# Performance work log

Hardware: AMD Instinct MI355X
Metric: run time of the kernel (lower is better)

## Reference

```python
import jax, jax.numpy as jnp
import numpy as np

B, T, N, H, F, E = 8, 64, 2048, 64, 64, 32768
G = 3 * H  # GRU gate dim


def setup_inputs() -> dict:
    key = jax.random.key(0)
    ks = jax.random.split(key, 12)
    s = 0.05
    return {
        "x": jax.random.normal(ks[0], (B, T, N, F), jnp.float32),
        "targets": jax.random.normal(ks[1], (B, T, N, 1), jnp.float32),
        "targets_mask": jax.random.uniform(ks[2], (B, T, N, 1)) > 0.2,
        "edge_index": jax.random.randint(ks[3], (2, E), 0, N),
        "W_msg": jax.random.normal(ks[4], (H, H), jnp.float32) * s,
        "b_msg": jnp.zeros((H,), jnp.float32),
        "W_mix": jax.random.normal(ks[5], (H, H + F), jnp.float32) * s,
        "b_mix": jnp.zeros((H,), jnp.float32),
        "W_ih": jax.random.normal(ks[6], (N, G, H), jnp.float32) * s,
        "W_hh": jax.random.normal(ks[7], (N, G, H), jnp.float32) * s,
        "b_ih": jnp.zeros((N, G), jnp.float32),
        "b_hh": jnp.zeros((N, G), jnp.float32),
        "W_read": jax.random.normal(ks[8], (1, H), jnp.float32) * s,
        "b_read": jnp.zeros((1,), jnp.float32),
    }


def reference(x, targets, targets_mask, edge_index,
              W_msg, b_msg, W_mix, b_mix,
              W_ih, W_hh, b_ih, b_hh, W_read, b_read):
    src, dst = edge_index[0], edge_index[1]

    def step(state, x_t):
        # state: [B,N,H], x_t: [B,N,F]
        m = jnp.einsum('bnh,gh->bng', state, W_msg) + b_msg           # state_to_message
        agg = jnp.zeros_like(m).at[:, dst, :].add(m[:, src, :])       # add-aggregate over directed edges
        mi = jnp.concatenate([agg, x_t], axis=-1)                     # [B,N,H+F]
        m2 = jnp.einsum('bnf,hf->bnh', mi, W_mix) + b_mix             # mix_input
        # per-node independent GRU cells (batched weights [N,3H,*])
        gi = jnp.einsum('bnh,ngh->bng', m2, W_ih) + b_ih
        gh = jnp.einsum('bnh,ngh->bng', state, W_hh) + b_hh
        i_r, i_z, i_n = jnp.split(gi, 3, axis=-1)
        h_r, h_z, h_n = jnp.split(gh, 3, axis=-1)
        r = jax.nn.sigmoid(i_r + h_r)
        z = jax.nn.sigmoid(i_z + h_z)
        n_cand = jnp.tanh(i_n + r * h_n)
        new_state = (1.0 - z) * n_cand + z * state
        out = jnp.einsum('bnh,oh->bno', new_state, W_read) + b_read   # readout -> [B,N,1]
        return new_state, out

    state0 = jnp.zeros((B, N, H), x.dtype)
    _, outs = jax.lax.scan(step, state0, jnp.swapaxes(x, 0, 1))       # outs: [T,B,N,1]
    outputs = jnp.swapaxes(outs, 0, 1)                                # [B,T,N,1]
    loss = 0.5 * (outputs - targets) ** 2
    mask = targets_mask.astype(loss.dtype)
    return jnp.sum(loss * mask) / jnp.sum(mask)                       # masked mean
```

## Files before the change

kernel.cpp:

```cpp
#include <hip/hip_runtime.h>
#include <math.h>

namespace {
constexpr int B = 8, T = 64, N = 2048, H = 64, F = 64, E = 32768, G = 192;
constexpr int BNH = B * N * H;
constexpr int NWELEM = N * G * H;
constexpr int NBLK = 1024;
}

typedef __attribute__((ext_vector_type(8))) short bfrag;
typedef __attribute__((ext_vector_type(4))) float ffrag;
typedef long f8frag;

#define MFMA(a, b, c)  __builtin_amdgcn_mfma_f32_16x16x32_bf16(a, b, c, 0, 0, 0)
#define MFMA8(a, b, c) __builtin_amdgcn_mfma_f32_16x16x32_fp8_fp8(a, b, c, 0, 0, 0)

#define DS (1.f / 512.f)

__device__ __forceinline__ unsigned short f2bf(float f) {
  unsigned u = __float_as_uint(f);
  u += 0x7fffu + ((u >> 16) & 1u);
  return (unsigned short)(u >> 16);
}
__device__ __forceinline__ float bf2f(unsigned short u) {
  return __uint_as_float(((unsigned)u) << 16);
}
template<bool HI>
__device__ __forceinline__ unsigned cvtpk8(float a, float b, unsigned old) {
  return __builtin_amdgcn_cvt_pk_fp8_f32(a, b, old, HI);
}

__device__ __forceinline__ void grid_bar(int* bar, int t) {
  __syncthreads();
  if (threadIdx.x == 0) {
    __threadfence();
    int old = __hip_atomic_fetch_add(&bar[(blockIdx.x & 63) * 64], 1,
                                     __ATOMIC_RELAXED, __HIP_MEMORY_SCOPE_AGENT);
    if ((old & 15) == 15) {
      int old2 = __hip_atomic_fetch_add(&bar[4096], 1,
                                        __ATOMIC_RELAXED, __HIP_MEMORY_SCOPE_AGENT);
      if ((old2 & 63) == 63)
        __hip_atomic_fetch_add(&bar[4160], 1, __ATOMIC_RELAXED, __HIP_MEMORY_SCOPE_AGENT);
    }
    while (__hip_atomic_load(&bar[4160], __ATOMIC_RELAXED, __HIP_MEMORY_SCOPE_AGENT) <= t)
      __builtin_amdgcn_s_sleep(8);
    __threadfence();
  }
  __syncthreads();
}


__global__ __launch_bounds__(256) void init_kernel(
    float* __restrict__ state, unsigned short* __restrict__ mA,
    const float* __restrict__ b_msg, float* __restrict__ loss_acc,
    float* __restrict__ scal, int* __restrict__ deg, int* __restrict__ bar)
{
  int stride = gridDim.x * blockDim.x;
  for (int i = blockIdx.x * blockDim.x + threadIdx.x; i < BNH; i += stride) {
    state[i] = 0.f;
    mA[i] = f2bf(b_msg[i & (H - 1)]);
    if (i < 8192) bar[i] = 0;
    if (i < N) { loss_acc[i] = 0.f; deg[i] = 0; }
    if (i < 16) scal[i] = 0.f;
  }
}

__global__ __launch_bounds__(256) void conv_kernel(
    const float* __restrict__ Wi, const float* __restrict__ Wh,
    const float* __restrict__ Wm, const float* __restrict__ Wg,
    unsigned char* __restrict__ Wib, unsigned char* __restrict__ Whb,
    unsigned short* __restrict__ Wmb, unsigned short* __restrict__ Wgb)
{
  int stride = gridDim.x * blockDim.x * 2;
  for (int i = (blockIdx.x * blockDim.x + threadIdx.x) * 2; i < NWELEM; i += stride) {
    unsigned p = cvtpk8<false>(Wi[i] * 32.f, Wi[i + 1] * 32.f, 0u);
    *(unsigned short*)(Wib + i) = (unsigned short)p;
    p = cvtpk8<false>(Wh[i] * 32.f, Wh[i + 1] * 32.f, 0u);
    *(unsigned short*)(Whb + i) = (unsigned short)p;
    if (i < 64 * 128) { Wmb[i] = f2bf(Wm[i]); Wmb[i + 1] = f2bf(Wm[i + 1]); }
    if (i < 64 * 64)  { Wgb[i] = f2bf(Wg[i]); Wgb[i + 1] = f2bf(Wg[i + 1]); }
  }
}

__global__ __launch_bounds__(256) void hist_kernel(const int* __restrict__ ei, int* __restrict__ deg) {
  int e = blockIdx.x * 256 + threadIdx.x;
  if (e < E) atomicAdd(&deg[ei[E + e]], 1);
}

__global__ __launch_bounds__(1024) void scan_kernel(const int* __restrict__ deg,
    int* __restrict__ row_ptr, int* __restrict__ cursor)
{
  __shared__ int s[N];
  int tid = threadIdx.x;
  s[tid] = deg[tid];
  s[tid + 1024] = deg[tid + 1024];
  __syncthreads();
  for (int off = 1; off < N; off <<= 1) {
    int v0 = (tid >= off) ? s[tid - off] : 0;
    int v1 = s[tid + 1024 - off];
    __syncthreads();
    s[tid] += v0;
    s[tid + 1024] += v1;
    __syncthreads();
  }
  row_ptr[tid + 1] = s[tid];
  row_ptr[tid + 1025] = s[tid + 1024];
  cursor[tid] = (tid == 0) ? 0 : s[tid - 1];
  cursor[tid + 1024] = s[tid + 1023];
  if (tid == 0) row_ptr[0] = 0;
}

__global__ __launch_bounds__(256) void fill_kernel(const int* __restrict__ ei,
    int* __restrict__ cursor, int* __restrict__ col_src)
{
  int e = blockIdx.x * 256 + threadIdx.x;
  if (e < E) {
    int d = ei[E + e];
    int slot = atomicAdd(&cursor[d], 1);
    col_src[slot] = ei[e];
  }
}

__global__ __launch_bounds__(256) void mask_kernel(const int* __restrict__ mask, float* __restrict__ scal) {
  int stride = gridDim.x * blockDim.x;
  int v = 0;
  for (int i = blockIdx.x * blockDim.x + threadIdx.x; i < B * T * N; i += stride)
    v += (mask[i] != 0);
  for (int o = 1; o < 64; o <<= 1) v += __shfl_xor(v, o, 64);
  if ((threadIdx.x & 63) == 0) atomicAdd(&scal[0], (float)v);
}


__global__ __attribute__((amdgpu_flat_work_group_size(256, 256), amdgpu_waves_per_eu(4, 4)))
void persist_kernel(
    const float* __restrict__ x, const float* __restrict__ targets,
    const int* __restrict__ mask,
    const unsigned char* __restrict__ W_ihb, const unsigned char* __restrict__ W_hhb,
    const unsigned short* __restrict__ W_mixb, const unsigned short* __restrict__ W_msgb,
    const float* __restrict__ b_ih, const float* __restrict__ b_hh,
    const float* __restrict__ b_mix, const float* __restrict__ b_msg,
    const float* __restrict__ W_read, const float* __restrict__ b_read,
    const int* __restrict__ row_ptr, const int* __restrict__ col_src,
    unsigned short* __restrict__ mAb, unsigned short* __restrict__ mBb,
    float* __restrict__ loss_acc, int* __restrict__ bar)
{
  __shared__ float sts[2][8][64];
  __shared__ float partial[4][8][72];
  __shared__ unsigned char m2F8[8 * 80];
  __shared__ unsigned short nsA[8 * 72];
  __shared__ float redS[4][8];

  const int tid = threadIdx.x;
  const int w = tid >> 6, lane = tid & 63;
  const int mrow = lane & 15, quad = lane >> 4;
  const int n0 = blockIdx.x * 2;
  const bfrag za = (bfrag)0;
  const int hcol = w * 16 + mrow;

  f8frag whf[2][6], wif[2][6];
#pragma unroll
  for (int k = 0; k < 2; ++k) {
    const unsigned char* Wh = W_hhb + (size_t)(n0 + k) * (G * H);
    const unsigned char* Wi = W_ihb + (size_t)(n0 + k) * (G * H);
#pragma unroll
    for (int tt = 0; tt < 3; ++tt) {
      const int off = ((w + tt * 4) * 16 + mrow) * H + quad * 8;
      whf[k][2 * tt]     = *(const f8frag*)(Wh + off);
      whf[k][2 * tt + 1] = *(const f8frag*)(Wh + off + 32);
      wif[k][2 * tt]     = *(const f8frag*)(Wi + off);
      wif[k][2 * tt + 1] = *(const f8frag*)(Wi + off + 32);
    }
  }
  const unsigned short* wmp = W_mixb + hcol * 128 + quad * 8;
  const unsigned short* wgp = W_msgb + hcol * H + quad * 8;

  float bir[2], biz[2], bin_[2], bhr[2], bhz[2], bhn[2];
#pragma unroll
  for (int k = 0; k < 2; ++k) {
    const int bg = (n0 + k) * G + hcol;
    bir[k] = b_ih[bg]; biz[k] = b_ih[bg + 64]; bin_[k] = b_ih[bg + 128];
    bhr[k] = b_hh[bg]; bhz[k] = b_hh[bg + 64]; bhn[k] = b_hh[bg + 128];
  }
  float wrd = W_read[hcol];
  float bmix = b_mix[hcol];
  float bmsg = b_msg[hcol];
  const float brd = b_read[0];
  const int e0a = row_ptr[n0], e0b = row_ptr[n0 + 1], e0c = row_ptr[n0 + 2];

#pragma unroll
  for (int k = 0; k < 2; ++k) {
#pragma unroll
    for (int j = 0; j < 6; ++j) {
      asm volatile("" : "+v"(whf[k][j]));
      asm volatile("" : "+v"(wif[k][j]));
    }
    asm volatile("" : "+v"(bir[k]), "+v"(biz[k]), "+v"(bin_[k]),
                      "+v"(bhr[k]), "+v"(bhz[k]), "+v"(bhn[k]));
  }
  asm volatile("" : "+v"(wrd), "+v"(bmix), "+v"(bmsg));

  for (int i = tid; i < 2 * 8 * 64; i += 256) ((float*)sts)[i] = 0.f;
  __syncthreads();

  float lsum[2] = {0.f, 0.f};
  unsigned short* mcur = mAb;
  unsigned short* mnxt = mBb;

#pragma unroll 1
  for (int t = 0; t < T; ++t) {
#pragma unroll
    for (int k = 0; k < 2; ++k) {
      const int nn = n0 + k;
      const int ee0 = k ? e0b : e0a;
      const int ee1 = k ? e0c : e0b;

      bfrag wm0 = *(const bfrag*)(wmp);
      bfrag wm1 = *(const bfrag*)(wmp + 32);
      bfrag wm2 = *(const bfrag*)(wmp + 64);
      bfrag wm3 = *(const bfrag*)(wmp + 96);
      f8frag asF0 = 0, asF1 = 0;
      bfrag a2 = za, a3 = za;
      if (mrow < 8) {
        const float* sp = &sts[k][mrow][0];
        {
          float4 s0 = *(const float4*)(sp + quad * 8);
          float4 s1 = *(const float4*)(sp + quad * 8 + 4);
          unsigned u0 = 0, u1 = 0;
          u0 = cvtpk8<false>(s0.x * 16.f, s0.y * 16.f, u0);
          u0 = cvtpk8<true >(s0.z * 16.f, s0.w * 16.f, u0);
          u1 = cvtpk8<false>(s1.x * 16.f, s1.y * 16.f, u1);
          u1 = cvtpk8<true >(s1.z * 16.f, s1.w * 16.f, u1);
          asF0 = (f8frag)(((unsigned long long)u1 << 32) | u0);
          s0 = *(const float4*)(sp + 32 + quad * 8);
          s1 = *(const float4*)(sp + 32 + quad * 8 + 4);
          u0 = 0; u1 = 0;
          u0 = cvtpk8<false>(s0.x * 16.f, s0.y * 16.f, u0);
          u0 = cvtpk8<true >(s0.z * 16.f, s0.w * 16.f, u0);
          u1 = cvtpk8<false>(s1.x * 16.f, s1.y * 16.f, u1);
          u1 = cvtpk8<true >(s1.z * 16.f, s1.w * 16.f, u1);
          asF1 = (f8frag)(((unsigned long long)u1 << 32) | u0);
        }
        const float* xp = x + (((size_t)mrow * T + t) * N + nn) * F;
        {
          float4 t0 = *(const float4*)(xp + quad * 8);
          float4 t1 = *(const float4*)(xp + quad * 8 + 4);
          a2[0]=(short)f2bf(t0.x); a2[1]=(short)f2bf(t0.y); a2[2]=(short)f2bf(t0.z); a2[3]=(short)f2bf(t0.w);
          a2[4]=(short)f2bf(t1.x); a2[5]=(short)f2bf(t1.y); a2[6]=(short)f2bf(t1.z); a2[7]=(short)f2bf(t1.w);
          t0 = *(const float4*)(xp + 32 + quad * 8);
          t1 = *(const float4*)(xp + 32 + quad * 8 + 4);
          a3[0]=(short)f2bf(t0.x); a3[1]=(short)f2bf(t0.y); a3[2]=(short)f2bf(t0.z); a3[3]=(short)f2bf(t0.w);
          a3[4]=(short)f2bf(t1.x); a3[5]=(short)f2bf(t1.y); a3[6]=(short)f2bf(t1.z); a3[7]=(short)f2bf(t1.w);
        }
      }
      {
        float acc[8] = {0.f,0.f,0.f,0.f,0.f,0.f,0.f,0.f};
#pragma unroll 2
        for (int e = ee0 + w; e < ee1; e += 4) {
          const unsigned short* mp = mcur + (size_t)col_src[e] * (B * H) + lane;
#pragma unroll
          for (int b = 0; b < 8; ++b) acc[b] += bf2f(mp[b * H]);
        }
#pragma unroll
        for (int b = 0; b < 8; ++b) partial[w][b][lane] = acc[b];
      }
      ffrag ah0 = {0.f,0.f,0.f,0.f}, ah1 = {0.f,0.f,0.f,0.f}, ah2 = {0.f,0.f,0.f,0.f};
      ah0 = MFMA8(asF0, whf[k][0], ah0); ah0 = MFMA8(asF1, whf[k][1], ah0);
      ah1 = MFMA8(asF0, whf[k][2], ah1); ah1 = MFMA8(asF1, whf[k][3], ah1);
      ah2 = MFMA8(asF0, whf[k][4], ah2); ah2 = MFMA8(asF1, whf[k][5], ah2);
      __syncthreads();

      {
        bfrag a0 = za, a1 = za;
        if (mrow < 8) {
          const float* p = &partial[0][mrow][quad * 8];
#pragma unroll
          for (int j = 0; j < 8; ++j) {
            float s = p[j] + p[j + 576] + p[j + 1152] + p[j + 1728];
            a0[j] = (short)f2bf(s);
          }
          const float* p2 = &partial[0][mrow][32 + quad * 8];
#pragma unroll
          for (int j = 0; j < 8; ++j) {
            float s = p2[j] + p2[j + 576] + p2[j + 1152] + p2[j + 1728];
            a1[j] = (short)f2bf(s);
          }
        }
        ffrag accm = {0.f, 0.f, 0.f, 0.f};
        accm = MFMA(a0, wm0, accm);
        accm = MFMA(a1, wm1, accm);
        accm = MFMA(a2, wm2, accm);
        accm = MFMA(a3, wm3, accm);
        if (quad < 2) {
#pragma unroll
          for (int r = 0; r < 4; ++r) {
            unsigned p = cvtpk8<false>((accm[r] + bmix) * 16.f, 0.f, 0u);
            m2F8[(quad * 4 + r) * 80 + hcol] = (unsigned char)(p & 0xffu);
          }
        }
      }
      __syncthreads();

      bfrag wg0 = *(const bfrag*)(wgp);
      bfrag wg1 = *(const bfrag*)(wgp + 32);
      {
        f8frag amF0 = 0, amF1 = 0;
        if (mrow < 8) {
          amF0 = *(const f8frag*)&m2F8[mrow * 80 + quad * 8];
          amF1 = *(const f8frag*)&m2F8[mrow * 80 + 32 + quad * 8];
        }
        ffrag ai0 = {0.f,0.f,0.f,0.f}, ai1 = {0.f,0.f,0.f,0.f}, ai2 = {0.f,0.f,0.f,0.f};
        ai0 = MFMA8(amF0, wif[k][0], ai0); ai0 = MFMA8(amF1, wif[k][1], ai0);
        ai1 = MFMA8(amF0, wif[k][2], ai1); ai1 = MFMA8(amF1, wif[k][3], ai1);
        ai2 = MFMA8(amF0, wif[k][4], ai2); ai2 = MFMA8(amF1, wif[k][5], ai2);
        if (quad < 2) {
          float v[4];
#pragma unroll
          for (int r = 0; r < 4; ++r) {
            const int b = quad * 4 + r;
            float rs  = (ai0[r] + ah0[r]) * DS + bir[k] + bhr[k];
            float zs  = (ai1[r] + ah1[r]) * DS + biz[k] + bhz[k];
            float in_ = ai2[r] * DS + bin_[k];
            float hn  = ah2[r] * DS + bhn[k];
            float rg = 1.f / (1.f + __expf(-rs));
            float z  = 1.f / (1.f + __expf(-zs));
            float pre = in_ + rg * hn;
            float a = __expf(-2.f * fabsf(pre));
            float nc = copysignf((1.f - a) / (1.f + a), pre);
            float sold = sts[k][b][hcol];
            float ns = (1.f - z) * nc + z * sold;
            sts[k][b][hcol] = ns;
            nsA[b * 72 + hcol] = f2bf(ns);
            v[r] = ns * wrd;
          }
#pragma unroll
          for (int o = 1; o < 16; o <<= 1) {
#pragma unroll
            for (int r = 0; r < 4; ++r) v[r] += __shfl_xor(v[r], o, 64);
          }
          if (mrow == 0) {
#pragma unroll
            for (int r = 0; r < 4; ++r) redS[w][quad * 4 + r] = v[r];
          }
        }
      }
      __syncthreads();

      {
        bfrag an0 = za, an1 = za;
        if (mrow < 8) {
          an0 = *(const bfrag*)&nsA[mrow * 72 + quad * 8];
          an1 = *(const bfrag*)&nsA[mrow * 72 + 32 + quad * 8];
        }
        ffrag accg = {0.f, 0.f, 0.f, 0.f};
        accg = MFMA(an0, wg0, accg);
        accg = MFMA(an1, wg1, accg);
        if (quad < 2) {
#pragma unroll
          for (int r = 0; r < 4; ++r)
            mnxt[(size_t)nn * (B * H) + (quad * 4 + r) * H + hcol] = f2bf(accg[r] + bmsg);
        }
      }
      if (tid < 8) {
        float vv = redS[0][tid] + redS[1][tid] + redS[2][tid] + redS[3][tid] + brd;
        size_t idx = ((size_t)tid * T + t) * N + nn;
        float d = vv - targets[idx];
        float l = (mask[idx] != 0) ? 0.5f * d * d : 0.f;
        l += __shfl_xor(l, 1, 64);
        l += __shfl_xor(l, 2, 64);
        l += __shfl_xor(l, 4, 64);
        if (tid == 0) lsum[k] += l;
      }
    }
    grid_bar(bar, t);
    unsigned short* tp = mcur; mcur = mnxt; mnxt = tp;
  }
  if (tid == 0) { loss_acc[n0] = lsum[0]; loss_acc[n0 + 1] = lsum[1]; }
}


__global__ __launch_bounds__(256, 4) void step_kernel(
    const float* __restrict__ x, const float* __restrict__ targets,
    const int* __restrict__ mask, float* __restrict__ state,
    const unsigned char* __restrict__ W_ihb, const unsigned char* __restrict__ W_hhb,
    const unsigned short* __restrict__ W_mixb, const unsigned short* __restrict__ W_msgb,
    const float* __restrict__ b_ih, const float* __restrict__ b_hh,
    const float* __restrict__ b_mix, const float* __restrict__ b_msg,
    const float* __restrict__ W_read, const float* __restrict__ b_read,
    const int* __restrict__ row_ptr, const int* __restrict__ col_src,
    const unsigned short* __restrict__ m_cur, unsigned short* __restrict__ m_nxt,
    float* __restrict__ loss_acc, int t)
{
  __shared__ float partial[4][8][72];
  __shared__ unsigned char m2F8[8 * 80];
  __shared__ unsigned short nsA[8 * 72];
  __shared__ float redS[4][8];

  const int n = blockIdx.x;
  const int tid = threadIdx.x;
  const int w = tid >> 6, lane = tid & 63;
  const int mrow = lane & 15, quad = lane >> 4;
  const bfrag za = (bfrag)0;

  f8frag whf[6];
  {
    const unsigned char* Wh = W_hhb + (size_t)n * (G * H);
#pragma unroll
    for (int tt = 0; tt < 3; ++tt) {
      const unsigned char* wrh = Wh + (((w + tt * 4) * 16 + mrow) * H) + quad * 8;
      whf[2 * tt]     = *(const f8frag*)(wrh);
      whf[2 * tt + 1] = *(const f8frag*)(wrh + 32);
    }
  }
  f8frag asF0 = 0, asF1 = 0;
  float4 xv0 = {0.f,0.f,0.f,0.f}, xv1 = {0.f,0.f,0.f,0.f};
  float4 xv2 = {0.f,0.f,0.f,0.f}, xv3 = {0.f,0.f,0.f,0.f};
  if (mrow < 8) {
    const float* sp = state + (size_t)n * (B * H) + mrow * H;
    float4 s0 = *(const float4*)(sp + quad * 8);
    float4 s1 = *(const float4*)(sp + quad * 8 + 4);
    float4 s2 = *(const float4*)(sp + 32 + quad * 8);
    float4 s3 = *(const float4*)(sp + 32 + quad * 8 + 4);
    unsigned u0 = 0, u1 = 0;
    u0 = cvtpk8<false>(s0.x * 16.f, s0.y * 16.f, u0);
    u0 = cvtpk8<true >(s0.z * 16.f, s0.w * 16.f, u0);
    u1 = cvtpk8<false>(s1.x * 16.f, s1.y * 16.f, u1);
    u1 = cvtpk8<true >(s1.z * 16.f, s1.w * 16.f, u1);
    asF0 = (f8frag)(((unsigned long long)u1 << 32) | u0);
    u0 = 0; u1 = 0;
    u0 = cvtpk8<false>(s2.x * 16.f, s2.y * 16.f, u0);
    u0 = cvtpk8<true >(s2.z * 16.f, s2.w * 16.f, u0);
    u1 = cvtpk8<false>(s3.x * 16.f, s3.y * 16.f, u1);
    u1 = cvtpk8<true >(s3.z * 16.f, s3.w * 16.f, u1);
    asF1 = (f8frag)(((unsigned long long)u1 << 32) | u0);
    const float* xp = x + (((size_t)mrow * T + t) * N + n) * F;
    xv0 = *(const float4*)(xp + quad * 8);
    xv1 = *(const float4*)(xp + quad * 8 + 4);
    xv2 = *(const float4*)(xp + 32 + quad * 8);
    xv3 = *(const float4*)(xp + 32 + quad * 8 + 4);
  }
  {
    float acc[8] = {0.f,0.f,0.f,0.f,0.f,0.f,0.f,0.f};
    const int e0 = row_ptr[n], e1 = row_ptr[n + 1];
#pragma unroll 2
    for (int e = e0 + w; e < e1; e += 4) {
      const unsigned short* mp = m_cur + (size_t)col_src[e] * (B * H) + lane;
#pragma unroll
      for (int b = 0; b < 8; ++b) acc[b] += bf2f(mp[b * H]);
    }
#pragma unroll
    for (int b = 0; b < 8; ++b) partial[w][b][lane] = acc[b];
  }
  ffrag ah0 = {0.f,0.f,0.f,0.f}, ah1 = {0.f,0.f,0.f,0.f}, ah2 = {0.f,0.f,0.f,0.f};
  ah0 = MFMA8(asF0, whf[0], ah0); ah0 = MFMA8(asF1, whf[1], ah0);
  ah1 = MFMA8(asF0, whf[2], ah1); ah1 = MFMA8(asF1, whf[3], ah1);
  ah2 = MFMA8(asF0, whf[4], ah2); ah2 = MFMA8(asF1, whf[5], ah2);
  __syncthreads();

  f8frag wif[6];
  {
    const unsigned char* Wi = W_ihb + (size_t)n * (G * H);
#pragma unroll
    for (int tt = 0; tt < 3; ++tt) {
      const unsigned char* wri = Wi + (((w + tt * 4) * 16 + mrow) * H) + quad * 8;
      wif[2 * tt]     = *(const f8frag*)(wri);
      wif[2 * tt + 1] = *(const f8frag*)(wri + 32);
    }
  }
  {
    const int g0 = w * 16;
    bfrag a0 = za, a1 = za, a2 = za, a3 = za;
    if (mrow < 8) {
      const float* p = &partial[0][mrow][quad * 8];
#pragma unroll
      for (int j = 0; j < 8; ++j) {
        float s = p[j] + p[j + 576] + p[j + 1152] + p[j + 1728];
        a0[j] = (short)f2bf(s);
      }
      const float* p2 = &partial[0][mrow][32 + quad * 8];
#pragma unroll
      for (int j = 0; j < 8; ++j) {
        float s = p2[j] + p2[j + 576] + p2[j + 1152] + p2[j + 1728];
        a1[j] = (short)f2bf(s);
      }
      a2[0]=(short)f2bf(xv0.x); a2[1]=(short)f2bf(xv0.y); a2[2]=(short)f2bf(xv0.z); a2[3]=(short)f2bf(xv0.w);
      a2[4]=(short)f2bf(xv1.x); a2[5]=(short)f2bf(xv1.y); a2[6]=(short)f2bf(xv1.z); a2[7]=(short)f2bf(xv1.w);
      a3[0]=(short)f2bf(xv2.x); a3[1]=(short)f2bf(xv2.y); a3[2]=(short)f2bf(xv2.z); a3[3]=(short)f2bf(xv2.w);
      a3[4]=(short)f2bf(xv3.x); a3[5]=(short)f2bf(xv3.y); a3[6]=(short)f2bf(xv3.z); a3[7]=(short)f2bf(xv3.w);
    }
    const unsigned short* wm = W_mixb + (g0 + mrow) * 128 + quad * 8;
    ffrag accm = {0.f, 0.f, 0.f, 0.f};
    accm = MFMA(a0, *(const bfrag*)(wm), accm);
    accm = MFMA(a1, *(const bfrag*)(wm + 32), accm);
    accm = MFMA(a2, *(const bfrag*)(wm + 64), accm);
    accm = MFMA(a3, *(const bfrag*)(wm + 96), accm);
    if (quad < 2) {
      float bm = b_mix[g0 + mrow];
#pragma unroll
      for (int r = 0; r < 4; ++r) {
        unsigned p = cvtpk8<false>((accm[r] + bm) * 16.f, 0.f, 0u);
        m2F8[(quad * 4 + r) * 80 + g0 + mrow] = (unsigned char)(p & 0xffu);
      }
    }
  }
  __syncthreads();

  {
    f8frag amF0 = 0, amF1 = 0;
    if (mrow < 8) {
      amF0 = *(const f8frag*)&m2F8[mrow * 80 + quad * 8];
      amF1 = *(const f8frag*)&m2F8[mrow * 80 + 32 + quad * 8];
    }
    ffrag ai0 = {0.f,0.f,0.f,0.f}, ai1 = {0.f,0.f,0.f,0.f}, ai2 = {0.f,0.f,0.f,0.f};
    ai0 = MFMA8(amF0, wif[0], ai0); ai0 = MFMA8(amF1, wif[1], ai0);
    ai1 = MFMA8(amF0, wif[2], ai1); ai1 = MFMA8(amF1, wif[3], ai1);
    ai2 = MFMA8(amF0, wif[4], ai2); ai2 = MFMA8(amF1, wif[5], ai2);
    if (quad < 2) {
      const int hcol = w * 16 + mrow;
      const int bg = n * G + hcol;
      const float bir = b_ih[bg], biz = b_ih[bg + 64], bin_ = b_ih[bg + 128];
      const float bhr = b_hh[bg], bhz = b_hh[bg + 64], bhn = b_hh[bg + 128];
      const float wrd = W_read[hcol];
      float v[4];
#pragma unroll
      for (int r = 0; r < 4; ++r) {
        const int b = quad * 4 + r;
        float rs  = (ai0[r] + ah0[r]) * DS + bir + bhr;
        float zs  = (ai1[r] + ah1[r]) * DS + biz + bhz;
        float in_ = ai2[r] * DS + bin_;
        float hn  = ah2[r] * DS + bhn;
        float rg = 1.f / (1.f + __expf(-rs));
        float z  = 1.f / (1.f + __expf(-zs));
        float pre = in_ + rg * hn;
        float a = __expf(-2.f * fabsf(pre));
        float nc = copysignf((1.f - a) / (1.f + a), pre);
        float sold = state[(size_t)n * (B * H) + b * H + hcol];
        float ns = (1.f - z) * nc + z * sold;
        state[(size_t)n * (B * H) + b * H + hcol] = ns;
        nsA[b * 72 + hcol] = f2bf(ns);
        v[r] = ns * wrd;
      }
#pragma unroll
      for (int o = 1; o < 16; o <<= 1) {
#pragma unroll
        for (int r = 0; r < 4; ++r) v[r] += __shfl_xor(v[r], o, 64);
      }
      if (mrow == 0) {
#pragma unroll
        for (int r = 0; r < 4; ++r) redS[w][quad * 4 + r] = v[r];
      }
    }
  }
  __syncthreads();

  {
    const int g0 = w * 16;
    bfrag an0 = za, an1 = za;
    if (mrow < 8) {
      an0 = *(const bfrag*)&nsA[mrow * 72 + quad * 8];
      an1 = *(const bfrag*)&nsA[mrow * 72 + 32 + quad * 8];
    }
    const unsigned short* wg = W_msgb + (g0 + mrow) * H + quad * 8;
    ffrag accg = {0.f, 0.f, 0.f, 0.f};
    accg = MFMA(an0, *(const bfrag*)(wg), accg);
    accg = MFMA(an1, *(const bfrag*)(wg + 32), accg);
    if (quad < 2) {
      float bm = b_msg[g0 + mrow];
#pragma unroll
      for (int r = 0; r < 4; ++r)
        m_nxt[(size_t)n * (B * H) + (quad * 4 + r) * H + g0 + mrow] = f2bf(accg[r] + bm);
    }
  }
  if (tid < 8) {
    float vv = redS[0][tid] + redS[1][tid] + redS[2][tid] + redS[3][tid] + b_read[0];
    size_t idx = ((size_t)tid * T + t) * N + n;
    float d = vv - targets[idx];
    float l = (mask[idx] != 0) ? 0.5f * d * d : 0.f;
    l += __shfl_xor(l, 1, 64);
    l += __shfl_xor(l, 2, 64);
    l += __shfl_xor(l, 4, 64);
    if (tid == 0) loss_acc[n] += l;
  }
}

__global__ __launch_bounds__(256) void final_kernel(const float* __restrict__ loss_acc,
    const float* __restrict__ scal, float* __restrict__ out)
{
  __shared__ float sred[4];
  float v = 0.f;
  for (int i = threadIdx.x; i < N; i += 256) v += loss_acc[i];
  for (int o = 1; o < 64; o <<= 1) v += __shfl_xor(v, o, 64);
  if ((threadIdx.x & 63) == 0) sred[threadIdx.x >> 6] = v;
  __syncthreads();
  if (threadIdx.x == 0) out[0] = (sred[0] + sred[1] + sred[2] + sred[3]) / scal[0];
}

extern "C" void kernel_launch(void* const* d_in, const int* in_sizes, int n_in,
                              void* d_out, int out_size, void* d_ws, size_t ws_size,
                              hipStream_t stream)
{
  const float* x       = (const float*)d_in[0];
  const float* targets = (const float*)d_in[1];
  const int*   mask    = (const int*)d_in[2];
  const int*   ei      = (const int*)d_in[3];
  const float* W_msg   = (const float*)d_in[4];
  const float* b_msg   = (const float*)d_in[5];
  const float* W_mix   = (const float*)d_in[6];
  const float* b_mix   = (const float*)d_in[7];
  const float* W_ih    = (const float*)d_in[8];
  const float* W_hh    = (const float*)d_in[9];
  const float* b_ih    = (const float*)d_in[10];
  const float* b_hh    = (const float*)d_in[11];
  const float* W_read  = (const float*)d_in[12];
  const float* b_read  = (const float*)d_in[13];
  float* out = (float*)d_out;

  float* state          = (float*)d_ws;
  unsigned short* mA    = (unsigned short*)(state + BNH);
  unsigned short* mB    = mA + BNH;
  float* loss_acc       = (float*)(mB + BNH);
  float* scal           = loss_acc + N;
  int* deg              = (int*)(scal + 16);
  int* row_ptr          = deg + N;
  int* cursor           = row_ptr + (N + 16);
  int* col_src          = cursor + N;
  int* bar              = col_src + E;
  unsigned char* W_ihb  = (unsigned char*)(bar + 8192);
  unsigned char* W_hhb  = W_ihb + NWELEM;
  unsigned short* W_mixb = (unsigned short*)(W_hhb + NWELEM);
  unsigned short* W_msgb = W_mixb + 64 * 128;

  init_kernel<<<1024, 256, 0, stream>>>(state, mA, b_msg, loss_acc, scal, deg, bar);
  conv_kernel<<<8192, 256, 0, stream>>>(W_ih, W_hh, W_mix, W_msg, W_ihb, W_hhb, W_mixb, W_msgb);
  hist_kernel<<<E / 256, 256, 0, stream>>>(ei, deg);
  scan_kernel<<<1, 1024, 0, stream>>>(deg, row_ptr, cursor);
  fill_kernel<<<E / 256, 256, 0, stream>>>(ei, cursor, col_src);
  mask_kernel<<<512, 256, 0, stream>>>(mask, scal);

  int dev = 0, ncu = 0, occ = 0;
  hipGetDevice(&dev);
  hipDeviceGetAttribute(&ncu, hipDeviceAttributeMultiprocessorCount, dev);
  hipOccupancyMaxActiveBlocksPerMultiprocessor(&occ, (const void*)persist_kernel, 256, 0);
  const bool use_persist = ((long)occ * ncu >= NBLK);

  if (use_persist) {
    persist_kernel<<<NBLK, 256, 0, stream>>>(x, targets, mask,
                                             W_ihb, W_hhb, W_mixb, W_msgb,
                                             b_ih, b_hh, b_mix, b_msg, W_read, b_read,
                                             row_ptr, col_src, mA, mB, loss_acc, bar);
  } else {
    unsigned short* mcur = mA;
    unsigned short* mnxt = mB;
    for (int t = 0; t < T; ++t) {
      step_kernel<<<N, 256, 0, stream>>>(x, targets, mask, state,
                                         W_ihb, W_hhb, W_mixb, W_msgb,
                                         b_ih, b_hh, b_mix, b_msg, W_read, b_read,
                                         row_ptr, col_src, mcur, mnxt, loss_acc, t);
      unsigned short* tmp = mcur; mcur = mnxt; mnxt = tmp;
    }
  }
  final_kernel<<<1, 256, 0, stream>>>(loss_acc, scal, out);
}
```

Measured before the change: 2.223 ms.

## Replace hierarchical grid barrier with master-block barrier and packed atomic message accesses

Replaces the tree-style atomic grid barrier, which used thread fences and a two-level counter, with release-ordered per-slot counters. Block 0 polls all 64 slots and publishes a single generation flag, which the other blocks spin on with short sleeps. Message gather and scatter now use 32-bit packed bf16 pairs through relaxed agent-scope atomic loads and stores, presumably so the data stays coherent without full fences and with fewer, wider memory accesses. This risks weaker memory-ordering guarantees, since there is no acquire fence after the wait, and adds a serial polling step in block 0.

New measurement: 2.221 ms. No clear change (-0.1%).

```diff
diff --git a/kernel.cpp b/kernel.cpp
--- a/kernel.cpp
+++ b/kernel.cpp
@@ -33,18 +33,20 @@
 __device__ __forceinline__ void grid_bar(int* bar, int t) {
   __syncthreads();
   if (threadIdx.x == 0) {
-    __threadfence();
-    int old = __hip_atomic_fetch_add(&bar[(blockIdx.x & 63) * 64], 1,
-                                     __ATOMIC_RELAXED, __HIP_MEMORY_SCOPE_AGENT);
-    if ((old & 15) == 15) {
-      int old2 = __hip_atomic_fetch_add(&bar[4096], 1,
-                                        __ATOMIC_RELAXED, __HIP_MEMORY_SCOPE_AGENT);
-      if ((old2 & 63) == 63)
-        __hip_atomic_fetch_add(&bar[4160], 1, __ATOMIC_RELAXED, __HIP_MEMORY_SCOPE_AGENT);
-    }
-    while (__hip_atomic_load(&bar[4160], __ATOMIC_RELAXED, __HIP_MEMORY_SCOPE_AGENT) <= t)
-      __builtin_amdgcn_s_sleep(8);
-    __threadfence();
+    __hip_atomic_fetch_add(&bar[(blockIdx.x & 63) * 16], 1,
+                           __ATOMIC_RELEASE, __HIP_MEMORY_SCOPE_AGENT);
+  }
+  if (blockIdx.x == 0) {
+    if (threadIdx.x < 64) {
+      while (__hip_atomic_load(&bar[threadIdx.x * 16],
+                               __ATOMIC_RELAXED, __HIP_MEMORY_SCOPE_AGENT) < 16 * (t + 1))
+        __builtin_amdgcn_s_sleep(1);
+      if (threadIdx.x == 0)
+        __hip_atomic_store(&bar[4096], t + 1, __ATOMIC_RELAXED, __HIP_MEMORY_SCOPE_AGENT);
+    }
+  } else if (threadIdx.x == 0) {
+    while (__hip_atomic_load(&bar[4096], __ATOMIC_RELAXED, __HIP_MEMORY_SCOPE_AGENT) < t + 1)
+      __builtin_amdgcn_s_sleep(2);
   }
   __syncthreads();
 }
@@ -253,15 +255,24 @@
         }
       }
       {
-        float acc[8] = {0.f,0.f,0.f,0.f,0.f,0.f,0.f,0.f};
-#pragma unroll 2
+        float accL[4] = {0.f,0.f,0.f,0.f}, accH[4] = {0.f,0.f,0.f,0.f};
+        const int j = lane & 31, bh = lane >> 5;
+        const unsigned* mcU = (const unsigned*)mcur;
         for (int e = ee0 + w; e < ee1; e += 4) {
-          const unsigned short* mp = mcur + (size_t)col_src[e] * (B * H) + lane;
-#pragma unroll
-          for (int b = 0; b < 8; ++b) acc[b] += bf2f(mp[b * H]);
-        }
-#pragma unroll
-        for (int b = 0; b < 8; ++b) partial[w][b][lane] = acc[b];
+          const unsigned* mp = mcU + (size_t)col_src[e] * 256 + bh * 32 + j;
+#pragma unroll
+          for (int bb = 0; bb < 4; ++bb) {
+            unsigned v = __hip_atomic_load(mp + bb * 64, __ATOMIC_RELAXED,
+                                           __HIP_MEMORY_SCOPE_AGENT);
+            accL[bb] += bf2f((unsigned short)(v & 0xffffu));
+            accH[bb] += bf2f((unsigned short)(v >> 16));
+          }
+        }
+#pragma unroll
+        for (int bb = 0; bb < 4; ++bb) {
+          partial[w][bb * 2 + bh][2 * j]     = accL[bb];
+          partial[w][bb * 2 + bh][2 * j + 1] = accH[bb];
+        }
       }
       ffrag ah0 = {0.f,0.f,0.f,0.f}, ah1 = {0.f,0.f,0.f,0.f}, ah2 = {0.f,0.f,0.f,0.f};
       ah0 = MFMA8(asF0, whf[k][0], ah0); ah0 = MFMA8(asF1, whf[k][1], ah0);
@@ -355,9 +366,18 @@
         accg = MFMA(an0, wg0, accg);
         accg = MFMA(an1, wg1, accg);
         if (quad < 2) {
-#pragma unroll
-          for (int r = 0; r < 4; ++r)
-            mnxt[(size_t)nn * (B * H) + (quad * 4 + r) * H + hcol] = f2bf(accg[r] + bmsg);
+          unsigned* mnU = (unsigned*)mnxt;
+          const int jcol = hcol >> 1;
+#pragma unroll
+          for (int r = 0; r < 4; ++r) {
+            float v0 = accg[r] + bmsg;
+            float v1 = __shfl_xor(v0, 1, 64);
+            if (!(mrow & 1)) {
+              unsigned pk = (unsigned)f2bf(v0) | ((unsigned)f2bf(v1) << 16);
+              __hip_atomic_store(&mnU[(size_t)nn * 256 + (quad * 4 + r) * 32 + jcol],
+                                 pk, __ATOMIC_RELAXED, __HIP_MEMORY_SCOPE_AGENT);
+            }
+          }
         }
       }
       if (tid < 8) {
```
